# Kernel tuning notes

Measured on AMD Instinct MI355X. Metric: run time of the kernel, lower is better.

Reference implementation:

```python
import jax, jax.numpy as jnp
import numpy as np

MAX_DEPTH = 7
DEPTH_SIZES = [4 ** d for d in range(1, MAX_DEPTH + 1)]  # nodes per depth
N_NODES = sum(DEPTH_SIZES)  # 21844
N_TIMES = 48
HIDDEN = 1024
ENC_DIM = 256
B, S = 128, 32


def setup_inputs() -> dict:
    key = jax.random.key(0)
    k = jax.random.split(key, 6)
    return {
        "prefix_embedding": jax.random.normal(k[0], (B, S, HIDDEN), dtype=jnp.float32),
        "emb_matrix": jax.random.normal(k[1], (N_NODES, ENC_DIM), dtype=jnp.float32) * 0.02,
        "W_key": jax.random.normal(k[2], (HIDDEN, ENC_DIM), dtype=jnp.float32) * (1.0 / np.sqrt(ENC_DIM)),
        "b_key": jax.random.normal(k[3], (HIDDEN,), dtype=jnp.float32) * 0.01,
        "W_time": jax.random.normal(k[4], (N_TIMES, HIDDEN), dtype=jnp.float32) * (1.0 / np.sqrt(HIDDEN)),
        "b_time": jax.random.normal(k[5], (N_TIMES,), dtype=jnp.float32) * 0.01,
    }


def reference(prefix_embedding, emb_matrix, W_key, b_key, W_time, b_time):
    # keys = embedding_to_key(make_embedding_matrix(...)): [N_NODES, HIDDEN]
    keys = emb_matrix @ W_key.T + b_key
    # bmm(prefix [B,S,H], keys^T): keys identical across batch -> shared einsum
    scores = jnp.einsum("bsh,nh->bsn", prefix_embedding, keys)  # [B,S,N_NODES]
    # multitask: per-depth gather of the contiguous node block + log_softmax
    locations = []
    off = 0
    for n in DEPTH_SIZES:
        locations.append(jax.nn.log_softmax(scores[..., off:off + n], axis=-1))
        off += n
    time = jax.nn.log_softmax(prefix_embedding @ W_time.T + b_time, axis=-1)  # [B,S,N_TIMES]
    return tuple(locations) + (time,)
```

## Files before the change

kernel.cpp:

```cpp
#include <hip/hip_runtime.h>

#define NNODES 21844
#define ENC 256
#define HID 1024
#define ROWS 4096
#define NTIMES 48

typedef __attribute__((ext_vector_type(8))) short bf16x8;
typedef __attribute__((ext_vector_type(4))) float f32x4;

__device__ const int g_off[8] = {0, 4, 20, 84, 340, 1364, 5460, 21844};
__device__ const int g_l2[7]  = {2, 4, 6, 8, 10, 12, 14};

__device__ inline unsigned short f2bf(float f) {
  unsigned int u = __float_as_uint(f);
  u += 0x7FFF + ((u >> 16) & 1);
  return (unsigned short)(u >> 16);
}

__device__ inline int depth_of(int c) {
  return (c >= 4) + (c >= 20) + (c >= 84) + (c >= 340) + (c >= 1364) + (c >= 5460);
}

__global__ __launch_bounds__(256) void prep(const float* __restrict__ prefix,
                                            const float* __restrict__ emb,
                                            const float* __restrict__ Wk,
                                            const float* __restrict__ Wt,
                                            unsigned short* __restrict__ Pb16,
                                            unsigned short* __restrict__ Eb,
                                            unsigned short* __restrict__ WkT,
                                            float* __restrict__ WtT) {
  int bid = blockIdx.x, tid = threadIdx.x;
  if (bid < 4096) {
    int i = bid * 256 + tid;
    float4 v = reinterpret_cast<const float4*>(prefix)[i];
    ushort4 o; o.x = f2bf(v.x); o.y = f2bf(v.y); o.z = f2bf(v.z); o.w = f2bf(v.w);
    reinterpret_cast<ushort4*>(Pb16)[i] = o;
  } else if (bid < 9557) {
    int i = (bid - 4096) * 256 + tid;
    float4 v = reinterpret_cast<const float4*>(emb)[i];
    ushort4 o; o.x = f2bf(v.x); o.y = f2bf(v.y); o.z = f2bf(v.z); o.w = f2bf(v.w);
    reinterpret_cast<ushort4*>(Eb)[i] = o;
  } else if (bid < 10581) {
    int i = (bid - 9557) * 256 + tid;
    int e = i >> 10, h = i & 1023;
    WkT[i] = f2bf(Wk[h * ENC + e]);
  } else {
    int i = (bid - 10581) * 256 + tid;
    int k = i / NTIMES, c = i % NTIMES;
    WtT[i] = Wt[c * HID + k];
  }
}

__global__ __launch_bounds__(256) void p2_mfma(const unsigned short* __restrict__ Ab,
                                               const unsigned short* __restrict__ Bb,
                                               unsigned short* __restrict__ P2) {
  int lane = threadIdx.x & 63, w = threadIdx.x >> 6;
  int lr = lane & 15, lg = lane >> 4;
  int m0 = blockIdx.y * 64 + w * 16;
  int nb = blockIdx.x * 64;
  f32x4 acc[4];
#pragma unroll
  for (int n = 0; n < 4; ++n) acc[n] = f32x4{0.f, 0.f, 0.f, 0.f};
  const unsigned short* Ap = Ab + (long)(m0 + lr) * HID + lg * 8;
  for (int kk = 0; kk < 32; ++kk) {
    bf16x8 a = *reinterpret_cast<const bf16x8*>(Ap + kk * 32);
#pragma unroll
    for (int n = 0; n < 4; ++n) {
      bf16x8 b = *reinterpret_cast<const bf16x8*>(Bb + (long)(nb + n * 16 + lr) * HID + kk * 32 + lg * 8);
      acc[n] = __builtin_amdgcn_mfma_f32_16x16x32_bf16(a, b, acc[n], 0, 0, 0);
    }
  }
#pragma unroll
  for (int n = 0; n < 4; ++n)
#pragma unroll
    for (int j = 0; j < 4; ++j)
      P2[(m0 + lg * 4 + j) * ENC + nb + n * 16 + lr] = f2bf(acc[n][j]);
}

#define GEMM_TILE_BODY                                                                     \
  __shared__ unsigned short As[128 * 64];                                                  \
  __shared__ unsigned short Bs[128 * 64];                                                  \
  int tid = threadIdx.x;                                                                   \
  int lane = tid & 63, w = tid >> 6;                                                       \
  int lr = lane & 15, lg = lane >> 4;                                                      \
  int wr = w >> 1, wc = w & 1;                                                             \
  int m0 = blockIdx.x * 128, n0 = blockIdx.y * 128;                                        \
  int rr = tid >> 3, c8 = tid & 7;                                                         \
  f32x4 acc[4][4];                                                                         \
  _Pragma("unroll") for (int m = 0; m < 4; ++m)                                            \
    _Pragma("unroll") for (int n = 0; n < 4; ++n) acc[m][n] = f32x4{0.f, 0.f, 0.f, 0.f};   \
  for (int kt = 0; kt < 4; ++kt) {                                                         \
    if (kt) __syncthreads();                                                               \
    _Pragma("unroll") for (int r = 0; r < 4; ++r) {                                        \
      const unsigned short* ga = P2 + (long)(m0 + r * 32 + rr) * ENC + kt * 64 + c8 * 8;   \
      __builtin_amdgcn_global_load_lds(                                                    \
          (const __attribute__((address_space(1))) unsigned int*)ga,                       \
          (__attribute__((address_space(3))) unsigned int*)(As + r * 2048 + w * 512),      \
          16, 0, 0);                                                                       \
      int er = n0 + r * 32 + rr;                                                           \
      if (er > NNODES - 1) er = NNODES - 1;                                                \
      const unsigned short* gb = E + (long)er * ENC + kt * 64 + c8 * 8;                    \
      __builtin_amdgcn_global_load_lds(                                                    \
          (const __attribute__((address_space(1))) unsigned int*)gb,                       \
          (__attribute__((address_space(3))) unsigned int*)(Bs + r * 2048 + w * 512),      \
          16, 0, 0);                                                                       \
    }                                                                                      \
    __syncthreads();                                                                       \
    _Pragma("unroll") for (int kk = 0; kk < 2; ++kk) {                                     \
      bf16x8 a[4], b[4];                                                                   \
      _Pragma("unroll") for (int m = 0; m < 4; ++m)                                        \
        a[m] = *reinterpret_cast<const bf16x8*>(As + (wr * 64 + m * 16 + lr) * 64 + kk * 32 + lg * 8); \
      _Pragma("unroll") for (int n = 0; n < 4; ++n)                                        \
        b[n] = *reinterpret_cast<const bf16x8*>(Bs + (wc * 64 + n * 16 + lr) * 64 + kk * 32 + lg * 8); \
      _Pragma("unroll") for (int m = 0; m < 4; ++m)                                        \
        _Pragma("unroll") for (int n = 0; n < 4; ++n)                                      \
          acc[m][n] = __builtin_amdgcn_mfma_f32_16x16x32_bf16(a[m], b[n], acc[m][n], 0, 0, 0); \
    }                                                                                      \
  }

__global__ __launch_bounds__(256) void gemm_lse(const unsigned short* __restrict__ P2,
                                                const unsigned short* __restrict__ E,
                                                float* __restrict__ S) {
  GEMM_TILE_BODY
  int rbase = m0 + wr * 64 + lg * 4;
  int hstart = n0 + wc * 64;
  int dlo = depth_of(hstart);
  int hend = hstart + 63; if (hend > NNODES - 1) hend = NNODES - 1;
  int dhi = depth_of(hend);
  int cd[4];
#pragma unroll
  for (int n = 0; n < 4; ++n) {
    int gc = hstart + n * 16 + lr;
    cd[n] = (gc < NNODES) ? depth_of(gc) : 99;
  }
#pragma unroll
  for (int m = 0; m < 4; ++m)
#pragma unroll
    for (int n = 0; n < 4; ++n)
#pragma unroll
      for (int j = 0; j < 4; ++j) acc[m][n][j] = __expf(acc[m][n][j]);
  for (int dt = dlo; dt <= dhi; ++dt) {
#pragma unroll
    for (int m = 0; m < 4; ++m) {
      float s[4] = {0.f, 0.f, 0.f, 0.f};
#pragma unroll
      for (int n = 0; n < 4; ++n) {
        bool use = (cd[n] == dt);
#pragma unroll
        for (int j = 0; j < 4; ++j) s[j] += use ? acc[m][n][j] : 0.f;
      }
#pragma unroll
      for (int j = 0; j < 4; ++j)
#pragma unroll
        for (int o = 1; o < 16; o <<= 1) s[j] += __shfl_xor(s[j], o);
      if (lr == 0) {
#pragma unroll
        for (int j = 0; j < 4; ++j)
          atomicAdd(&S[dt * ROWS + rbase + m * 16 + j], s[j]);
      }
    }
  }
}

__global__ __launch_bounds__(256) void lse_log(const float* __restrict__ S,
                                               float* __restrict__ L) {
  int i = blockIdx.x * 256 + threadIdx.x;
  L[i] = __logf(S[i]);
}

__global__ __launch_bounds__(256) void gemm_write(const unsigned short* __restrict__ P2,
                                                  const unsigned short* __restrict__ E,
                                                  const float* __restrict__ Lse,
                                                  float* __restrict__ out) {
  GEMM_TILE_BODY
  int rbase = m0 + wr * 64 + lg * 4;
  int hstart = n0 + wc * 64;
#pragma unroll
  for (int n = 0; n < 4; ++n) {
    int gc = hstart + n * 16 + lr;
    if (gc >= NNODES) continue;
    int d = depth_of(gc);
    long ob = ((long)g_off[d] << 12) + (gc - g_off[d]);
    int sh = g_l2[d];
    const float* lp = Lse + d * ROWS;
#pragma unroll
    for (int m = 0; m < 4; ++m)
#pragma unroll
      for (int j = 0; j < 4; ++j) {
        int row = rbase + m * 16 + j;
        out[ob + ((long)row << sh)] = acc[m][n][j] - lp[row];
      }
  }
}

__global__ __launch_bounds__(256) void time_head(const float* __restrict__ prefix,
                                                 const float* __restrict__ WtT,
                                                 const float* __restrict__ bt,
                                                 float* __restrict__ out) {
  int lane = threadIdx.x & 63;
  int row = blockIdx.x * 4 + (threadIdx.x >> 6);
  const float4* pr = reinterpret_cast<const float4*>(prefix + (long)row * HID);
  float acc = -3.4e38f;
  if (lane < NTIMES) {
    float a = 0.f;
#pragma unroll 4
    for (int q = 0; q < HID / 4; ++q) {
      float4 pv = pr[q];
      const float* wrow = WtT + q * 4 * NTIMES;
      a += pv.x * wrow[lane] + pv.y * wrow[NTIMES + lane] +
           pv.z * wrow[2 * NTIMES + lane] + pv.w * wrow[3 * NTIMES + lane];
    }
    acc = a + bt[lane];
  }
  float m = acc;
#pragma unroll
  for (int d = 32; d; d >>= 1) m = fmaxf(m, __shfl_xor(m, d));
  float e = (lane < NTIMES) ? __expf(acc - m) : 0.f;
  float s = e;
#pragma unroll
  for (int d = 32; d; d >>= 1) s += __shfl_xor(s, d);
  if (lane < NTIMES) out[89473024 + row * NTIMES + lane] = acc - m - __logf(s);
}

extern "C" void kernel_launch(void* const* d_in, const int* in_sizes, int n_in,
                              void* d_out, int out_size, void* d_ws, size_t ws_size,
                              hipStream_t stream) {
  const float* prefix = (const float*)d_in[0];
  const float* emb    = (const float*)d_in[1];
  const float* Wk     = (const float*)d_in[2];
  const float* Wt     = (const float*)d_in[4];
  const float* bt     = (const float*)d_in[5];
  float* out = (float*)d_out;
  char* ws = (char*)d_ws;

  unsigned short* P2   = (unsigned short*)(ws + 0);
  unsigned short* Eb   = (unsigned short*)(ws + 2097152);
  unsigned short* WkT  = (unsigned short*)(ws + 13281280);
  unsigned short* Pb16 = (unsigned short*)(ws + 13805568);
  float*          WtT  = (float*)(ws + 22194176);
  float*          S    = (float*)(ws + 22390784);
  float*          Lse  = (float*)(ws + 22505472);

  hipMemsetAsync(S, 0, 7 * ROWS * sizeof(float), stream);

  prep<<<10773, 256, 0, stream>>>(prefix, emb, Wk, Wt, Pb16, Eb, WkT, WtT);

  p2_mfma<<<dim3(4, 64), 256, 0, stream>>>(Pb16, WkT, P2);

  gemm_lse<<<dim3(32, 171), 256, 0, stream>>>(P2, Eb, S);

  lse_log<<<112, 256, 0, stream>>>(S, Lse);

  gemm_write<<<dim3(32, 171), 256, 0, stream>>>(P2, Eb, Lse, out);

  time_head<<<1024, 256, 0, stream>>>(prefix, WtT, bt, out);
}
```

Before: 366.8 us.

## Double-buffer GEMM LDS tiles, fold memset and log into other kernels

The shared GEMM tile body now uses two LDS buffers, so the global-to-LDS loads for the next K slice are issued while MFMAs run on the current one. The hipMemset of the sum buffer moves into extra blocks of the prep kernel. The lse_log kernel is removed and gemm_write computes __logf of the sums directly. time_head splits its dot product into four independent accumulators. Together these cut launches and hide load latency, at the cost of doubled LDS per block (possibly lower occupancy) and many redundant log evaluations in the output kernel.

```diff
diff --git a/kernel.cpp b/kernel.cpp
--- a/kernel.cpp
+++ b/kernel.cpp
@@ -10,7 +10,6 @@
 typedef __attribute__((ext_vector_type(4))) float f32x4;
 
 __device__ const int g_off[8] = {0, 4, 20, 84, 340, 1364, 5460, 21844};
-__device__ const int g_l2[7]  = {2, 4, 6, 8, 10, 12, 14};
 
 __device__ inline unsigned short f2bf(float f) {
   unsigned int u = __float_as_uint(f);
@@ -29,7 +28,8 @@
                                             unsigned short* __restrict__ Pb16,
                                             unsigned short* __restrict__ Eb,
                                             unsigned short* __restrict__ WkT,
-                                            float* __restrict__ WtT) {
+                                            float* __restrict__ WtT,
+                                            float* __restrict__ S) {
   int bid = blockIdx.x, tid = threadIdx.x;
   if (bid < 4096) {
     int i = bid * 256 + tid;
@@ -45,10 +45,13 @@
     int i = (bid - 9557) * 256 + tid;
     int e = i >> 10, h = i & 1023;
     WkT[i] = f2bf(Wk[h * ENC + e]);
-  } else {
+  } else if (bid < 10773) {
     int i = (bid - 10581) * 256 + tid;
     int k = i / NTIMES, c = i % NTIMES;
     WtT[i] = Wt[c * HID + k];
+  } else {
+    int i = (bid - 10773) * 256 + tid;
+    reinterpret_cast<float4*>(S)[i] = float4{0.f, 0.f, 0.f, 0.f};
   }
 }
 
@@ -78,45 +81,53 @@
       P2[(m0 + lg * 4 + j) * ENC + nb + n * 16 + lr] = f2bf(acc[n][j]);
 }
 
-#define GEMM_TILE_BODY                                                                     \
-  __shared__ unsigned short As[128 * 64];                                                  \
-  __shared__ unsigned short Bs[128 * 64];                                                  \
-  int tid = threadIdx.x;                                                                   \
-  int lane = tid & 63, w = tid >> 6;                                                       \
-  int lr = lane & 15, lg = lane >> 4;                                                      \
-  int wr = w >> 1, wc = w & 1;                                                             \
-  int m0 = blockIdx.x * 128, n0 = blockIdx.y * 128;                                        \
-  int rr = tid >> 3, c8 = tid & 7;                                                         \
-  f32x4 acc[4][4];                                                                         \
-  _Pragma("unroll") for (int m = 0; m < 4; ++m)                                            \
-    _Pragma("unroll") for (int n = 0; n < 4; ++n) acc[m][n] = f32x4{0.f, 0.f, 0.f, 0.f};   \
-  for (int kt = 0; kt < 4; ++kt) {                                                         \
-    if (kt) __syncthreads();                                                               \
-    _Pragma("unroll") for (int r = 0; r < 4; ++r) {                                        \
-      const unsigned short* ga = P2 + (long)(m0 + r * 32 + rr) * ENC + kt * 64 + c8 * 8;   \
-      __builtin_amdgcn_global_load_lds(                                                    \
-          (const __attribute__((address_space(1))) unsigned int*)ga,                       \
-          (__attribute__((address_space(3))) unsigned int*)(As + r * 2048 + w * 512),      \
-          16, 0, 0);                                                                       \
-      int er = n0 + r * 32 + rr;                                                           \
-      if (er > NNODES - 1) er = NNODES - 1;                                                \
-      const unsigned short* gb = E + (long)er * ENC + kt * 64 + c8 * 8;                    \
-      __builtin_amdgcn_global_load_lds(                                                    \
-          (const __attribute__((address_space(1))) unsigned int*)gb,                       \
-          (__attribute__((address_space(3))) unsigned int*)(Bs + r * 2048 + w * 512),      \
-          16, 0, 0);                                                                       \
-    }                                                                                      \
-    __syncthreads();                                                                       \
-    _Pragma("unroll") for (int kk = 0; kk < 2; ++kk) {                                     \
-      bf16x8 a[4], b[4];                                                                   \
-      _Pragma("unroll") for (int m = 0; m < 4; ++m)                                        \
-        a[m] = *reinterpret_cast<const bf16x8*>(As + (wr * 64 + m * 16 + lr) * 64 + kk * 32 + lg * 8); \
-      _Pragma("unroll") for (int n = 0; n < 4; ++n)                                        \
-        b[n] = *reinterpret_cast<const bf16x8*>(Bs + (wc * 64 + n * 16 + lr) * 64 + kk * 32 + lg * 8); \
-      _Pragma("unroll") for (int m = 0; m < 4; ++m)                                        \
-        _Pragma("unroll") for (int n = 0; n < 4; ++n)                                      \
-          acc[m][n] = __builtin_amdgcn_mfma_f32_16x16x32_bf16(a[m], b[n], acc[m][n], 0, 0, 0); \
-    }                                                                                      \
+#define GEMM_TILE_BODY                                                                    \
+  __shared__ unsigned short SH[2][2][128 * 64];                                           \
+  int tid = threadIdx.x;                                                                  \
+  int lane = tid & 63, w = tid >> 6;                                                      \
+  int lr = lane & 15, lg = lane >> 4;                                                     \
+  int wr = w >> 1, wc = w & 1;                                                            \
+  int m0 = blockIdx.x * 128, n0 = blockIdx.y * 128;                                       \
+  int rr = tid >> 3, c8 = tid & 7;                                                        \
+  f32x4 acc[4][4];                                                                        \
+  _Pragma("unroll") for (int m = 0; m < 4; ++m)                                           \
+    _Pragma("unroll") for (int n = 0; n < 4; ++n) acc[m][n] = f32x4{0.f, 0.f, 0.f, 0.f};  \
+  {                                                                                       \
+    STAGE(0, 0)                                                                           \
+    __syncthreads();                                                                      \
+    for (int kt = 0; kt < 4; ++kt) {                                                      \
+      int cur = kt & 1;                                                                   \
+      if (kt < 3) { STAGE(cur ^ 1, kt + 1) }                                              \
+      const unsigned short* As = &SH[cur][0][0];                                          \
+      const unsigned short* Bs = &SH[cur][1][0];                                          \
+      _Pragma("unroll") for (int kk = 0; kk < 2; ++kk) {                                  \
+        bf16x8 a[4], b[4];                                                                \
+        _Pragma("unroll") for (int m = 0; m < 4; ++m)                                     \
+          a[m] = *reinterpret_cast<const bf16x8*>(As + (wr * 64 + m * 16 + lr) * 64 + kk * 32 + lg * 8); \
+        _Pragma("unroll") for (int n = 0; n < 4; ++n)                                     \
+          b[n] = *reinterpret_cast<const bf16x8*>(Bs + (wc * 64 + n * 16 + lr) * 64 + kk * 32 + lg * 8); \
+        _Pragma("unroll") for (int m = 0; m < 4; ++m)                                     \
+          _Pragma("unroll") for (int n = 0; n < 4; ++n)                                   \
+            acc[m][n] = __builtin_amdgcn_mfma_f32_16x16x32_bf16(a[m], b[n], acc[m][n], 0, 0, 0); \
+      }                                                                                   \
+      __syncthreads();                                                                    \
+    }                                                                                     \
+  }
+
+#define STAGE(buf, kt)                                                                    \
+  _Pragma("unroll") for (int r = 0; r < 4; ++r) {                                         \
+    const unsigned short* ga = P2 + (long)(m0 + r * 32 + rr) * ENC + (kt) * 64 + c8 * 8;  \
+    __builtin_amdgcn_global_load_lds(                                                     \
+        (const __attribute__((address_space(1))) unsigned int*)ga,                        \
+        (__attribute__((address_space(3))) unsigned int*)(&SH[buf][0][r * 2048 + w * 512]), \
+        16, 0, 0);                                                                        \
+    int er = n0 + r * 32 + rr;                                                            \
+    if (er > NNODES - 1) er = NNODES - 1;                                                 \
+    const unsigned short* gb = E + (long)er * ENC + (kt) * 64 + c8 * 8;                   \
+    __builtin_amdgcn_global_load_lds(                                                     \
+        (const __attribute__((address_space(1))) unsigned int*)gb,                        \
+        (__attribute__((address_space(3))) unsigned int*)(&SH[buf][1][r * 2048 + w * 512]), \
+        16, 0, 0);                                                                        \
   }
 
 __global__ __launch_bounds__(256) void gemm_lse(const unsigned short* __restrict__ P2,
@@ -163,15 +174,9 @@
   }
 }
 
-__global__ __launch_bounds__(256) void lse_log(const float* __restrict__ S,
-                                               float* __restrict__ L) {
-  int i = blockIdx.x * 256 + threadIdx.x;
-  L[i] = __logf(S[i]);
-}
-
 __global__ __launch_bounds__(256) void gemm_write(const unsigned short* __restrict__ P2,
                                                   const unsigned short* __restrict__ E,
-                                                  const float* __restrict__ Lse,
+                                                  const float* __restrict__ S,
                                                   float* __restrict__ out) {
   GEMM_TILE_BODY
   int rbase = m0 + wr * 64 + lg * 4;
@@ -182,14 +187,14 @@
     if (gc >= NNODES) continue;
     int d = depth_of(gc);
     long ob = ((long)g_off[d] << 12) + (gc - g_off[d]);
-    int sh = g_l2[d];
-    const float* lp = Lse + d * ROWS;
+    int sh = 2 * (d + 1);
+    const float* sp = S + d * ROWS;
 #pragma unroll
     for (int m = 0; m < 4; ++m)
 #pragma unroll
       for (int j = 0; j < 4; ++j) {
         int row = rbase + m * 16 + j;
-        out[ob + ((long)row << sh)] = acc[m][n][j] - lp[row];
+        out[ob + ((long)row << sh)] = acc[m][n][j] - __logf(sp[row]);
       }
   }
 }
@@ -203,15 +208,16 @@
   const float4* pr = reinterpret_cast<const float4*>(prefix + (long)row * HID);
   float acc = -3.4e38f;
   if (lane < NTIMES) {
-    float a = 0.f;
-#pragma unroll 4
+    float a0 = 0.f, a1 = 0.f, a2 = 0.f, a3 = 0.f;
     for (int q = 0; q < HID / 4; ++q) {
       float4 pv = pr[q];
       const float* wrow = WtT + q * 4 * NTIMES;
-      a += pv.x * wrow[lane] + pv.y * wrow[NTIMES + lane] +
-           pv.z * wrow[2 * NTIMES + lane] + pv.w * wrow[3 * NTIMES + lane];
+      a0 += pv.x * wrow[lane];
+      a1 += pv.y * wrow[NTIMES + lane];
+      a2 += pv.z * wrow[2 * NTIMES + lane];
+      a3 += pv.w * wrow[3 * NTIMES + lane];
     }
-    acc = a + bt[lane];
+    acc = (a0 + a1) + (a2 + a3) + bt[lane];
   }
   float m = acc;
 #pragma unroll
@@ -234,25 +240,20 @@
   float* out = (float*)d_out;
   char* ws = (char*)d_ws;
 
-  unsigned short* P2   = (unsigned short*)(ws + 0);
-  unsigned short* Eb   = (unsigned short*)(ws + 2097152);
-  unsigned short* WkT  = (unsigned short*)(ws + 13281280);
-  unsigned short* Pb16 = (unsigned short*)(ws + 13805568);
-  float*          WtT  = (float*)(ws + 22194176);
-  float*          S    = (float*)(ws + 22390784);
-  float*          Lse  = (float*)(ws + 22505472);
-
-  hipMemsetAsync(S, 0, 7 * ROWS * sizeof(float), stream);
-
-  prep<<<10773, 256, 0, stream>>>(prefix, emb, Wk, Wt, Pb16, Eb, WkT, WtT);
+  unsigned short* P2    = (unsigned short*)(ws + 0);
+  unsigned short* Eb    = (unsigned short*)(ws + 2097152);
+  unsigned short* WkT   = (unsigned short*)(ws + 13281280);
+  unsigned short* Pb16  = (unsigned short*)(ws + 13805568);
+  float*          WtT   = (float*)(ws + 22194176);
+  float*          S     = (float*)(ws + 22390784);
+
+  prep<<<10801, 256, 0, stream>>>(prefix, emb, Wk, Wt, Pb16, Eb, WkT, WtT, S);
 
   p2_mfma<<<dim3(4, 64), 256, 0, stream>>>(Pb16, WkT, P2);
 
   gemm_lse<<<dim3(32, 171), 256, 0, stream>>>(P2, Eb, S);
 
-  lse_log<<<112, 256, 0, stream>>>(S, Lse);
-
-  gemm_write<<<dim3(32, 171), 256, 0, stream>>>(P2, Eb, Lse, out);
+  gemm_write<<<dim3(32, 171), 256, 0, stream>>>(P2, Eb, S, out);
 
   time_head<<<1024, 256, 0, stream>>>(prefix, WtT, bt, out);
 }
```

Measured after the change: 388.6 us. 6.0% more time.
